# Performance work log

Hardware: AMD Instinct MI355X
Metric: run time of the kernel (lower is better)

## Reference

```python
import jax, jax.numpy as jnp
import numpy as np

N = 16384          # nodes/edges
F = 128            # features per rank
L_MAX = 3
SIZES = [1, 3, 9, 27]   # 3^l components for l = 0..3

def _doublefactorial(n):
    x = 1
    for i in range(1, n + 1, 2):
        x *= i
    return x

def _factorial(n):
    x = 1
    for i in range(1, n + 1):
        x *= i
    return x

def _norm_l1l2l3(l1, l2, l3):
    # even-parity recoupling normalization (verbatim from source)
    J = l1 + l2 + l3
    J1 = J - 2 * l1 - 1
    J2 = J - 2 * l2 - 1
    J3 = J - 2 * l3 - 1
    num = (_factorial(l1) * _factorial(l2) * _doublefactorial(2 * l3 - 1)
           * _factorial((J1 + 1) // 2) * _factorial((J2 + 1) // 2))
    den = (_factorial(l3) * _doublefactorial(J1) * _doublefactorial(J2)
           * _doublefactorial(J3) * _factorial(J // 2))
    return num / den

# All even-parity recoupling paths (l1, l2, l3): triangle inequality + even l1+l2-l3.
PATHS = [(l1, l2, l3)
         for l3 in range(L_MAX + 1)
         for l1 in range(L_MAX + 1)
         for l2 in range(L_MAX + 1)
         if abs(l1 - l2) <= l3 <= l1 + l2 and (l1 + l2 - l3) % 2 == 0]
N_PATHS = len(PATHS)  # == 23 == _get_n_paths(3,3,3)

def setup_inputs() -> dict:
    key = jax.random.key(0)
    k1, k2, k3 = jax.random.split(key, 3)
    x = jax.random.normal(k1, (N, F * sum(SIZES)), dtype=jnp.float32)
    y = jax.random.normal(k2, (N, F * sum(SIZES)), dtype=jnp.float32)
    weights = jax.random.normal(k3, (N_PATHS, F), dtype=jnp.float32)
    return {"x": x, "y": y, "weights": weights}

def _split(t):
    # flat [N, F*40] -> list of [N, F, 3,...,3] (rank-l Cartesian blocks)
    blocks, off = [], 0
    for l, s in enumerate(SIZES):
        blocks.append(t[:, off:off + F * s].reshape((-1, F) + (3,) * l))
        off += F * s
    return blocks

def reference(x, y, weights):
    xs = _split(x)
    ys = _split(y)
    outs = [jnp.zeros((x.shape[0], F) + (3,) * l3, x.dtype) for l3 in range(L_MAX + 1)]
    for p, (l1, l2, l3) in enumerate(PATHS):
        k = (l1 + l2 - l3) // 2          # number of contracted Cartesian indices
        xa = 'abc'[:l1 - k]              # free indices from x
        c = 'uvw'[:k]                    # contracted indices
        yb = 'deg'[:l2 - k]              # free indices from y
        sub = f"nf{xa}{c},nf{c}{yb}->nf{xa}{yb}"
        z = jnp.einsum(sub, xs[l1], ys[l2])           # [N, F, 3^l3]
        w = weights[p].reshape((1, F) + (1,) * l3)    # per-path per-feature weight
        outs[l3] = outs[l3] + jnp.asarray(_norm_l1l2l3(l1, l2, l3), x.dtype) * w * z
    return jnp.concatenate([o.reshape(o.shape[0], -1) for o in outs], axis=1)
```

## Files before the change

### kernel.cpp

```cpp
#include <hip/hip_runtime.h>


#define FF 128
#define ROW 5120
#define QROW 1280

typedef float floatx4 __attribute__((ext_vector_type(4)));

__device__ __constant__ float NORMS[23] = {
    1.0f, 1.0f, 2.0f/3.0f, 0.4f,
    1.0f, 1.0f, 1.0f, 1.0f, 2.0f/3.0f, 2.0f/3.0f,
    1.0f, 0.75f, 1.0f, 1.0f, 1.0f, 1.0f, 0.75f,
    1.0f, 5.0f/9.0f, 5.0f/9.0f, 5.0f/6.0f, 1.0f, 5.0f/6.0f
};

#define GL2LDS(g, l)  __builtin_amdgcn_global_load_lds(                      \
        (const __attribute__((address_space(1))) void*)(g),                  \
        (__attribute__((address_space(3))) void*)(l), 16, 0, 0)

__global__ __launch_bounds__(64, 2) void wtp_kernel(
    const float* __restrict__ x, const float* __restrict__ y,
    const float* __restrict__ w, float* __restrict__ out)
{
    __shared__ float buf[2 * QROW];

    const int lane  = threadIdx.x;
    const int f     = lane & 31;
    const int h     = lane >> 5;
    const int n     = blockIdx.x >> 2;
    const int fbase = (blockIdx.x & 3) << 5;

    const float* xr = x + (size_t)n * ROW;
    const float* yr = y + (size_t)n * ROW;
    float* orow     = out + (size_t)n * ROW;

    int goff[5];
    #pragma unroll
    for (int i = 0; i < 5; ++i) {
        const int o = i * 256 + lane * 4;
        int r;
        if      (o < 32)  r = fbase         + o;
        else if (o < 128) r = 128  + fbase*3  + (o - 32);
        else if (o < 416) r = 512  + fbase*9  + (o - 128);
        else              r = 1664 + fbase*27 + (o - 416);
        goff[i] = r;
    }

    #pragma unroll
    for (int i = 0; i < 5; ++i) {
        GL2LDS(xr + goff[i], buf + i * 256);
        GL2LDS(yr + goff[i], buf + QROW + i * 256);
    }

    float c[23];
    #pragma unroll
    for (int p = 0; p < 23; ++p) c[p] = NORMS[p] * w[p * FF + fbase + f];

    asm volatile("s_waitcnt vmcnt(0)" ::: "memory");

    const float* bx = buf;
    const float* by = buf + QROW;
    const float x0 = bx[f], y0 = by[f];
    float x1[3], y1[3], x2[9], y2[9];
    #pragma unroll
    for (int j = 0; j < 3; ++j)  x1[j] = bx[32  + f*3 + j];
    #pragma unroll
    for (int j = 0; j < 3; ++j)  y1[j] = by[32  + f*3 + j];
    #pragma unroll
    for (int j = 0; j < 9; ++j)  x2[j] = bx[128 + f*9 + j];
    #pragma unroll
    for (int j = 0; j < 9; ++j)  y2[j] = by[128 + f*9 + j];

    const float* bx3 = bx + 416 + f*27;
    const float* by3 = by + 416 + f*27;

    float o0, o1[3], o2[9], o3[27];

    if (h == 0) {
        {
            float acc = c[0] * (x0 * y0);
            float d3 = 0.f;
            #pragma unroll
            for (int u = 0; u < 3; ++u) d3 += x1[u] * y1[u];
            acc += c[1] * d3;
            float d9 = 0.f;
            #pragma unroll
            for (int t = 0; t < 9; ++t) d9 += x2[t] * y2[t];
            acc += c[2] * d9;
            float d27 = 0.f;
            #pragma unroll
            for (int t = 0; t < 27; ++t) d27 += bx3[t] * by3[t];
            acc += c[3] * d27;
            o0 = acc;
        }
        #pragma unroll
        for (int d = 0; d < 3; ++d) {
            float acc = c[4] * (x0 * y1[d]) + c[5] * (x1[d] * y0);
            float s6 = 0.f, s7 = 0.f, s8 = 0.f, s9 = 0.f;
            #pragma unroll
            for (int u = 0; u < 3; ++u) s6 += x1[u] * y2[u*3 + d];
            #pragma unroll
            for (int u = 0; u < 3; ++u) s7 += x2[d*3 + u] * y1[u];
            #pragma unroll
            for (int t = 0; t < 9; ++t) s8 += x2[t] * by3[t*3 + d];
            #pragma unroll
            for (int t = 0; t < 9; ++t) s9 += bx3[d*9 + t] * y2[t];
            o1[d] = acc + c[6]*s6 + c[7]*s7 + c[8]*s8 + c[9]*s9;
        }
        #pragma unroll
        for (int t = 0; t < 9; ++t) {
            const int a = t / 3, d = t % 3;
            float acc = c[10] * (x0 * y2[t]) + c[11] * (x1[a] * y1[d])
                      + c[13] * (x2[t] * y0);
            float s12 = 0.f, s14 = 0.f, s15 = 0.f, s16 = 0.f;
            #pragma unroll
            for (int u = 0; u < 3; ++u) s12 += x1[u] * by3[u*9 + t];
            #pragma unroll
            for (int u = 0; u < 3; ++u) s14 += x2[a*3 + u] * y2[u*3 + d];
            #pragma unroll
            for (int u = 0; u < 3; ++u) s15 += bx3[t*3 + u] * y1[u];
            #pragma unroll
            for (int s = 0; s < 9; ++s) s16 += bx3[a*9 + s] * by3[s*3 + d];
            o2[t] = acc + c[12]*s12 + c[14]*s14 + c[15]*s15 + c[16]*s16;
        }
    } else {
        #pragma unroll
        for (int q = 0; q < 27; ++q) {
            const int a = q / 9, t9 = q % 9, r = q / 3, e = q % 3;
            float acc = c[17] * (x0 * by3[q]) + c[18] * (x1[a] * y2[t9])
                      + c[19] * (x2[r] * y1[e]) + c[21] * (bx3[q] * y0);
            float s20 = 0.f, s22 = 0.f;
            #pragma unroll
            for (int u = 0; u < 3; ++u) s20 += x2[a*3 + u] * by3[u*9 + t9];
            #pragma unroll
            for (int u = 0; u < 3; ++u) s22 += bx3[r*3 + u] * y2[u*3 + e];
            o3[q] = acc + c[20]*s20 + c[22]*s22;
        }
    }

    if (h == 0) {
        buf[f] = o0;
        #pragma unroll
        for (int d = 0; d < 3; ++d) buf[32  + f*3 + d] = o1[d];
        #pragma unroll
        for (int t = 0; t < 9; ++t) buf[128 + f*9 + t] = o2[t];
    } else {
        #pragma unroll
        for (int q = 0; q < 27; ++q) buf[416 + f*27 + q] = o3[q];
    }
    asm volatile("s_waitcnt lgkmcnt(0)" ::: "memory");
    __builtin_amdgcn_sched_barrier(0);

    #pragma unroll
    for (int i = 0; i < 5; ++i) {
        floatx4 v = *(const floatx4*)(buf + i * 256 + lane * 4);
        __builtin_nontemporal_store(v, (floatx4*)(orow + goff[i]));
    }
}

extern "C" void kernel_launch(void* const* d_in, const int* in_sizes, int n_in,
                              void* d_out, int out_size, void* d_ws, size_t ws_size,
                              hipStream_t stream) {
    const float* x = (const float*)d_in[0];
    const float* y = (const float*)d_in[1];
    const float* w = (const float*)d_in[2];
    float* out = (float*)d_out;

    const int n_nodes = in_sizes[0] / ROW;
    dim3 grid(n_nodes * 4), block(64);
    hipLaunchKernelGGL(wtp_kernel, grid, block, 0, stream, x, y, w, out);
}
```

Measured before the change: 201.6 us.

## Process chunks of nodes per block with double-buffered LDS prefetch

Each 64-thread block now loops over 32 consecutive nodes for its 32-feature slice instead of handling one node. While one node is computed, the next node's x/y rows are loaded asynchronously into a second LDS buffer, using counted vmcnt waits. The per-feature weight coefficients are loaded once per block rather than once per node, and the grid shrinks by the chunk factor. The cost is far fewer resident waves for hiding memory latency on a bandwidth-bound kernel, and the launch-bounds occupancy hint is dropped.

```diff
diff --git a/kernel.cpp b/kernel.cpp
--- a/kernel.cpp
+++ b/kernel.cpp
@@ -4,6 +4,7 @@
 #define FF 128
 #define ROW 5120
 #define QROW 1280
+#define CHUNK 32
 
 typedef float floatx4 __attribute__((ext_vector_type(4)));
 
@@ -18,21 +19,17 @@
         (const __attribute__((address_space(1))) void*)(g),                  \
         (__attribute__((address_space(3))) void*)(l), 16, 0, 0)
 
-__global__ __launch_bounds__(64, 2) void wtp_kernel(
+__global__ __launch_bounds__(64) void wtp_kernel(
     const float* __restrict__ x, const float* __restrict__ y,
     const float* __restrict__ w, float* __restrict__ out)
 {
-    __shared__ float buf[2 * QROW];
+    __shared__ float buf[2][2 * QROW];
 
     const int lane  = threadIdx.x;
     const int f     = lane & 31;
     const int h     = lane >> 5;
-    const int n     = blockIdx.x >> 2;
     const int fbase = (blockIdx.x & 3) << 5;
-
-    const float* xr = x + (size_t)n * ROW;
-    const float* yr = y + (size_t)n * ROW;
-    float* orow     = out + (size_t)n * ROW;
+    const int first = (blockIdx.x >> 2) * CHUNK;
 
     int goff[5];
     #pragma unroll
@@ -46,115 +43,143 @@
         goff[i] = r;
     }
 
-    #pragma unroll
-    for (int i = 0; i < 5; ++i) {
-        GL2LDS(xr + goff[i], buf + i * 256);
-        GL2LDS(yr + goff[i], buf + QROW + i * 256);
-    }
-
     float c[23];
     #pragma unroll
     for (int p = 0; p < 23; ++p) c[p] = NORMS[p] * w[p * FF + fbase + f];
-
     asm volatile("s_waitcnt vmcnt(0)" ::: "memory");
 
-    const float* bx = buf;
-    const float* by = buf + QROW;
-    const float x0 = bx[f], y0 = by[f];
-    float x1[3], y1[3], x2[9], y2[9];
-    #pragma unroll
-    for (int j = 0; j < 3; ++j)  x1[j] = bx[32  + f*3 + j];
-    #pragma unroll
-    for (int j = 0; j < 3; ++j)  y1[j] = by[32  + f*3 + j];
-    #pragma unroll
-    for (int j = 0; j < 9; ++j)  x2[j] = bx[128 + f*9 + j];
-    #pragma unroll
-    for (int j = 0; j < 9; ++j)  y2[j] = by[128 + f*9 + j];
-
-    const float* bx3 = bx + 416 + f*27;
-    const float* by3 = by + 416 + f*27;
-
-    float o0, o1[3], o2[9], o3[27];
-
-    if (h == 0) {
-        {
-            float acc = c[0] * (x0 * y0);
-            float d3 = 0.f;
-            #pragma unroll
-            for (int u = 0; u < 3; ++u) d3 += x1[u] * y1[u];
-            acc += c[1] * d3;
-            float d9 = 0.f;
-            #pragma unroll
-            for (int t = 0; t < 9; ++t) d9 += x2[t] * y2[t];
-            acc += c[2] * d9;
-            float d27 = 0.f;
-            #pragma unroll
-            for (int t = 0; t < 27; ++t) d27 += bx3[t] * by3[t];
-            acc += c[3] * d27;
-            o0 = acc;
-        }
+    {
+        const float* xr = x + (size_t)first * ROW;
+        const float* yr = y + (size_t)first * ROW;
         #pragma unroll
-        for (int d = 0; d < 3; ++d) {
-            float acc = c[4] * (x0 * y1[d]) + c[5] * (x1[d] * y0);
-            float s6 = 0.f, s7 = 0.f, s8 = 0.f, s9 = 0.f;
-            #pragma unroll
-            for (int u = 0; u < 3; ++u) s6 += x1[u] * y2[u*3 + d];
-            #pragma unroll
-            for (int u = 0; u < 3; ++u) s7 += x2[d*3 + u] * y1[u];
-            #pragma unroll
-            for (int t = 0; t < 9; ++t) s8 += x2[t] * by3[t*3 + d];
-            #pragma unroll
-            for (int t = 0; t < 9; ++t) s9 += bx3[d*9 + t] * y2[t];
-            o1[d] = acc + c[6]*s6 + c[7]*s7 + c[8]*s8 + c[9]*s9;
-        }
-        #pragma unroll
-        for (int t = 0; t < 9; ++t) {
-            const int a = t / 3, d = t % 3;
-            float acc = c[10] * (x0 * y2[t]) + c[11] * (x1[a] * y1[d])
-                      + c[13] * (x2[t] * y0);
-            float s12 = 0.f, s14 = 0.f, s15 = 0.f, s16 = 0.f;
-            #pragma unroll
-            for (int u = 0; u < 3; ++u) s12 += x1[u] * by3[u*9 + t];
-            #pragma unroll
-            for (int u = 0; u < 3; ++u) s14 += x2[a*3 + u] * y2[u*3 + d];
-            #pragma unroll
-            for (int u = 0; u < 3; ++u) s15 += bx3[t*3 + u] * y1[u];
-            #pragma unroll
-            for (int s = 0; s < 9; ++s) s16 += bx3[a*9 + s] * by3[s*3 + d];
-            o2[t] = acc + c[12]*s12 + c[14]*s14 + c[15]*s15 + c[16]*s16;
-        }
-    } else {
-        #pragma unroll
-        for (int q = 0; q < 27; ++q) {
-            const int a = q / 9, t9 = q % 9, r = q / 3, e = q % 3;
-            float acc = c[17] * (x0 * by3[q]) + c[18] * (x1[a] * y2[t9])
-                      + c[19] * (x2[r] * y1[e]) + c[21] * (bx3[q] * y0);
-            float s20 = 0.f, s22 = 0.f;
-            #pragma unroll
-            for (int u = 0; u < 3; ++u) s20 += x2[a*3 + u] * by3[u*9 + t9];
-            #pragma unroll
-            for (int u = 0; u < 3; ++u) s22 += bx3[r*3 + u] * y2[u*3 + e];
-            o3[q] = acc + c[20]*s20 + c[22]*s22;
+        for (int i = 0; i < 5; ++i) {
+            GL2LDS(xr + goff[i], &buf[0][i * 256]);
+            GL2LDS(yr + goff[i], &buf[0][QROW + i * 256]);
         }
     }
 
-    if (h == 0) {
-        buf[f] = o0;
+    int cur = 0;
+    for (int k = 0; k < CHUNK; ++k) {
+        const int node = first + k;
+
+        if (k + 1 < CHUNK) {
+            const float* xr = x + (size_t)(node + 1) * ROW;
+            const float* yr = y + (size_t)(node + 1) * ROW;
+            #pragma unroll
+            for (int i = 0; i < 5; ++i) {
+                GL2LDS(xr + goff[i], &buf[cur ^ 1][i * 256]);
+                GL2LDS(yr + goff[i], &buf[cur ^ 1][QROW + i * 256]);
+            }
+            if (k == 0) {
+                asm volatile("s_waitcnt vmcnt(10)" ::: "memory");
+            } else {
+                asm volatile("s_waitcnt vmcnt(15)" ::: "memory");
+            }
+        } else {
+            asm volatile("s_waitcnt vmcnt(5)" ::: "memory");
+        }
+
+        const float* bx = &buf[cur][0];
+        const float* by = &buf[cur][QROW];
+        const float x0 = bx[f], y0 = by[f];
+        float x1[3], y1[3], x2[9], y2[9];
         #pragma unroll
-        for (int d = 0; d < 3; ++d) buf[32  + f*3 + d] = o1[d];
+        for (int j = 0; j < 3; ++j)  x1[j] = bx[32  + f*3 + j];
         #pragma unroll
-        for (int t = 0; t < 9; ++t) buf[128 + f*9 + t] = o2[t];
-    } else {
+        for (int j = 0; j < 3; ++j)  y1[j] = by[32  + f*3 + j];
         #pragma unroll
-        for (int q = 0; q < 27; ++q) buf[416 + f*27 + q] = o3[q];
-    }
-    asm volatile("s_waitcnt lgkmcnt(0)" ::: "memory");
-    __builtin_amdgcn_sched_barrier(0);
+        for (int j = 0; j < 9; ++j)  x2[j] = bx[128 + f*9 + j];
+        #pragma unroll
+        for (int j = 0; j < 9; ++j)  y2[j] = by[128 + f*9 + j];
 
-    #pragma unroll
-    for (int i = 0; i < 5; ++i) {
-        floatx4 v = *(const floatx4*)(buf + i * 256 + lane * 4);
-        __builtin_nontemporal_store(v, (floatx4*)(orow + goff[i]));
+        const float* bx3 = bx + 416 + f*27;
+        const float* by3 = by + 416 + f*27;
+
+        float o0, o1[3], o2[9], o3[27];
+
+        if (h == 0) {
+            {
+                float acc = c[0] * (x0 * y0);
+                float d3 = 0.f;
+                #pragma unroll
+                for (int u = 0; u < 3; ++u) d3 += x1[u] * y1[u];
+                acc += c[1] * d3;
+                float d9 = 0.f;
+                #pragma unroll
+                for (int t = 0; t < 9; ++t) d9 += x2[t] * y2[t];
+                acc += c[2] * d9;
+                float d27 = 0.f;
+                #pragma unroll
+                for (int t = 0; t < 27; ++t) d27 += bx3[t] * by3[t];
+                acc += c[3] * d27;
+                o0 = acc;
+            }
+            #pragma unroll
+            for (int d = 0; d < 3; ++d) {
+                float acc = c[4] * (x0 * y1[d]) + c[5] * (x1[d] * y0);
+                float s6 = 0.f, s7 = 0.f, s8 = 0.f, s9 = 0.f;
+                #pragma unroll
+                for (int u = 0; u < 3; ++u) s6 += x1[u] * y2[u*3 + d];
+                #pragma unroll
+                for (int u = 0; u < 3; ++u) s7 += x2[d*3 + u] * y1[u];
+                #pragma unroll
+                for (int t = 0; t < 9; ++t) s8 += x2[t] * by3[t*3 + d];
+                #pragma unroll
+                for (int t = 0; t < 9; ++t) s9 += bx3[d*9 + t] * y2[t];
+                o1[d] = acc + c[6]*s6 + c[7]*s7 + c[8]*s8 + c[9]*s9;
+            }
+            #pragma unroll
+            for (int t = 0; t < 9; ++t) {
+                const int a = t / 3, d = t % 3;
+                float acc = c[10] * (x0 * y2[t]) + c[11] * (x1[a] * y1[d])
+                          + c[13] * (x2[t] * y0);
+                float s12 = 0.f, s14 = 0.f, s15 = 0.f, s16 = 0.f;
+                #pragma unroll
+                for (int u = 0; u < 3; ++u) s12 += x1[u] * by3[u*9 + t];
+                #pragma unroll
+                for (int u = 0; u < 3; ++u) s14 += x2[a*3 + u] * y2[u*3 + d];
+                #pragma unroll
+                for (int u = 0; u < 3; ++u) s15 += bx3[t*3 + u] * y1[u];
+                #pragma unroll
+                for (int s = 0; s < 9; ++s) s16 += bx3[a*9 + s] * by3[s*3 + d];
+                o2[t] = acc + c[12]*s12 + c[14]*s14 + c[15]*s15 + c[16]*s16;
+            }
+        } else {
+            #pragma unroll
+            for (int q = 0; q < 27; ++q) {
+                const int a = q / 9, t9 = q % 9, r = q / 3, e = q % 3;
+                float acc = c[17] * (x0 * by3[q]) + c[18] * (x1[a] * y2[t9])
+                          + c[19] * (x2[r] * y1[e]) + c[21] * (bx3[q] * y0);
+                float s20 = 0.f, s22 = 0.f;
+                #pragma unroll
+                for (int u = 0; u < 3; ++u) s20 += x2[a*3 + u] * by3[u*9 + t9];
+                #pragma unroll
+                for (int u = 0; u < 3; ++u) s22 += bx3[r*3 + u] * y2[u*3 + e];
+                o3[q] = acc + c[20]*s20 + c[22]*s22;
+            }
+        }
+
+        float* B = &buf[cur][0];
+        if (h == 0) {
+            B[f] = o0;
+            #pragma unroll
+            for (int d = 0; d < 3; ++d) B[32  + f*3 + d] = o1[d];
+            #pragma unroll
+            for (int t = 0; t < 9; ++t) B[128 + f*9 + t] = o2[t];
+        } else {
+            #pragma unroll
+            for (int q = 0; q < 27; ++q) B[416 + f*27 + q] = o3[q];
+        }
+        asm volatile("s_waitcnt lgkmcnt(0)" ::: "memory");
+        __builtin_amdgcn_sched_barrier(0);
+
+        float* orow = out + (size_t)node * ROW;
+        #pragma unroll
+        for (int i = 0; i < 5; ++i) {
+            floatx4 v = *(const floatx4*)(B + i * 256 + lane * 4);
+            __builtin_nontemporal_store(v, (floatx4*)(orow + goff[i]));
+        }
+        cur ^= 1;
     }
 }
 
@@ -167,6 +192,6 @@
     float* out = (float*)d_out;
 
     const int n_nodes = in_sizes[0] / ROW;
-    dim3 grid(n_nodes * 4), block(64);
+    dim3 grid((n_nodes / CHUNK) * 4), block(64);
     hipLaunchKernelGGL(wtp_kernel, grid, block, 0, stream, x, y, w, out);
 }
```

Measured after the change: 201.9 us. About the same (+0.2%).
